# Optimization experiments

Hardware: AMD Instinct MI355X
Metric: run time of the kernel (lower is better)

## Reference

```python
import jax, jax.numpy as jnp
import numpy as np

B, F0, D = 4096, 39, 16
CROSS_LAYER_SIZE = (128, 128)


def _he_uniform(key, shape):
    fan_in = int(np.prod(shape[:-1]))
    limit = np.sqrt(6.0 / fan_in)
    return jax.random.uniform(key, shape, jnp.float32, -limit, limit)


def setup_inputs() -> dict:
    key = jax.random.key(0)
    k_x, k_f0, k_f1, k_w, k_b = jax.random.split(key, 5)
    x = jax.random.normal(k_x, (B, F0, D), dtype=jnp.float32)
    # field_nums with direct=False: [39, 128//2=64, 64]
    f0 = _he_uniform(k_f0, (F0 * F0, CROSS_LAYER_SIZE[0]))          # (1521, 128)
    f1 = _he_uniform(k_f1, (F0 * (CROSS_LAYER_SIZE[0] // 2), CROSS_LAYER_SIZE[1]))  # (2496, 128)
    out_dim = CROSS_LAYER_SIZE[0] // 2 + CROSS_LAYER_SIZE[1]        # 192
    dense_w = _he_uniform(k_w, (out_dim, 1))
    dense_b = jnp.zeros((1,), dtype=jnp.float32)
    return {"x": x, "f0": f0, "f1": f1, "dense_w": dense_w, "dense_b": dense_b}


def reference(x, f0, f1, dense_w, dense_b):
    # CIN forward (direct=False, use_bias=False, use_residual=False, relu)
    # x: (B, F0, D)
    filters = [f0, f1]
    n_layers = len(CROSS_LAYER_SIZE)
    h = x  # hidden state, (B, Fk, D)
    finals = []
    for idx, L in enumerate(CROSS_LAYER_SIZE):
        Fk = h.shape[1]
        # filter f_ has shape (F0*Fk, L) with i (field of x0) major, j (field of h) minor
        Wr = filters[idx].reshape(F0, Fk, L)
        # fused outer product + conv1d (kernel width 1 == matmul over i,j):
        # z[b, m, d] = sum_{i,j} x[b,i,d] * h[b,j,d] * W[i,j,m]
        z = jnp.einsum('bid,bjd,ijm->bmd', x, h, Wr)  # (B, L, D)
        z = jax.nn.relu(z)
        if idx != n_layers - 1:
            # split along feature-map axis: first half feeds next layer,
            # second half goes to output
            h = z[:, : L // 2, :]
            finals.append(z[:, L // 2:, :])
        else:
            finals.append(z)
    result = jnp.sum(jnp.concatenate(finals, axis=1), axis=-1)  # (B, 192)
    return result @ dense_w + dense_b  # (B, 1)
```

## Files before the change

### kernel.cpp

```cpp
#include <hip/hip_runtime.h>


typedef _Float16 h2    __attribute__((ext_vector_type(2)));
typedef _Float16 f16x8 __attribute__((ext_vector_type(8)));
typedef __attribute__((ext_vector_type(16))) float f32x16;

#define XBB 1160
#define L0C 30
#define NCH 110

__device__ __constant__ int IG0[L0C] = {0,0,0,0,0, 1,1,1,1,1, 2,2,2,2, 3,3,3,3, 4,4,4, 5,5,5, 6,6, 7,7, 8, 9};
__device__ __constant__ int JG0[L0C] = {0,1,2,3,4, 0,1,2,3,4, 1,2,3,4, 1,2,3,4, 2,3,4, 2,3,4, 3,4, 3,4, 4, 4};
#define IG0T(c) ((c)<5?0:(c)<10?1:(c)<14?2:(c)<18?3:(c)<21?4:(c)<24?5:(c)<26?6:(c)<28?7:(c)<29?8:9)
#define JG0T(c) ((c)<10?((c)%5):(c)<18?(((c)-10)%4+1):(c)<24?(((c)-18)%3+2):(c)<28?(((c)-24)%2+3):4)

__global__ __launch_bounds__(256)
void CIN_repack(const float* __restrict__ f0, const float* __restrict__ f1,
                uint4* __restrict__ ws)
{
    const int tid  = blockIdx.x * 256 + threadIdx.x;
    const int n    = tid & 127;
    const int slot = tid >> 7;
    const int half = slot & 1;
    const int kh   = (slot >> 1) & 1;
    const int ch   = slot >> 2;
    float v[8];
    if (ch < L0C) {
        const int ig = IG0[ch], jg = JG0[ch];
        const int i = ig * 4 + kh * 2 + half;
#pragma unroll
        for (int t = 0; t < 8; ++t) {
            const int j = jg * 8 + t;
            float val = 0.f;
            if (i < 39 && j < 39 && j >= i) {
                val = f0[(i * 39 + j) * 128 + n];
                if (j > i) val += f0[(j * 39 + i) * 128 + n];
            }
            v[t] = val;
        }
    } else {
        const int c1 = ch - L0C;
        const int jg = c1 / 5, ig = c1 - jg * 5;
        const int j = jg * 4 + kh * 2 + half;
#pragma unroll
        for (int t = 0; t < 8; ++t) {
            const int i = ig * 8 + t;
            v[t] = (i < 39) ? f1[(i * 64 + j) * 128 + n] : 0.f;
        }
    }
    union { h2 h[4]; uint4 q; } pk;
#pragma unroll
    for (int t = 0; t < 4; ++t)
        pk.h[t] = h2{(_Float16)v[2 * t], (_Float16)v[2 * t + 1]};
    const int lane = half * 32 + (n & 31);
    const int cg   = n >> 5;
    ws[ch * 512 + kh * 256 + cg * 64 + lane] = pk.q;
}

__global__ __launch_bounds__(256, 4)
void CIN_main(const float* __restrict__ x,
              const char* __restrict__ wsB,
              const float* __restrict__ dw,
              const float* __restrict__ db,
              float* __restrict__ out)
{
    __shared__ __align__(16) _Float16 xsH[4 * XBB];
    __shared__ __align__(4)  _Float16 hsH[4][64][18];
    __shared__ float dws[192];
    __shared__ float red[4][4];

    const int tid  = threadIdx.x;
    const int w    = tid >> 6;
    const int lane = tid & 63;
    const int half = lane >> 5;
    const int d    = lane & 15;
    const int bsel = (lane >> 4) & 1;
    const int col  = lane & 31;

    const char* wbase = wsB + lane * 16 + w * 1024 + 2048;
    f16x8 Bb[2][2];
    auto loadBg = [&](int ch, f16x8 (&B)[2]) {
        const char* p0 = wbase + (size_t)ch * 8192;
        B[0] = *(const f16x8*)(p0 - 2048);
        B[1] = *(const f16x8*)(p0 + 2048);
    };

    loadBg(0, Bb[0]);
    loadBg(1, Bb[1]);

    const float4* xg4 = (const float4*)(x + (size_t)blockIdx.x * 4 * 624);
    for (int e4 = tid; e4 < 624; e4 += 256) {
        float4 v = xg4[e4];
        int bb = e4 / 156, r = e4 - bb * 156;
        int i = r >> 2, d0 = (r & 3) * 4;
        _Float16* bp = xsH + bb * XBB + i;
        bp[(d0 + 0) * 72] = (_Float16)v.x; bp[(d0 + 1) * 72] = (_Float16)v.y;
        bp[(d0 + 2) * 72] = (_Float16)v.z; bp[(d0 + 3) * 72] = (_Float16)v.w;
    }
    if (tid < 64) { int bb = tid >> 4, dd = tid & 15; xsH[bb * XBB + dd * 72 + 39] = (_Float16)0.f; }
    if (tid < 192) dws[tid] = dw[tid];
    __syncthreads();

    const _Float16* xrow[2] = {
        xsH + (0 * 2 + bsel) * XBB + d * 72,
        xsH + (1 * 2 + bsel) * XBB + d * 72
    };

    f32x16 acc[2];
#pragma unroll
    for (int p = 0; p < 2; ++p)
#pragma unroll
        for (int r = 0; r < 16; ++r) acc[p][r] = 0.f;

    h2 xiv2[2][2];

#pragma unroll
    for (int c = 0; c < L0C; ++c) {
        const int ig = IG0T(c);
        const int jg = JG0T(c);
        if ((c == 0) || (IG0T(c) != IG0T(c - 1))) {
#pragma unroll
            for (int p = 0; p < 2; ++p)
#pragma unroll
                for (int kh = 0; kh < 2; ++kh) {
                    _Float16 s = xrow[p][ig * 4 + kh * 2 + half];
                    xiv2[p][kh] = h2{s, s};
                }
        }
#pragma unroll
        for (int p = 0; p < 2; ++p) {
            union { f16x8 v; h2 h[4]; } xj;
            xj.v = *(const f16x8*)(xrow[p] + jg * 8);
            union { h2 h[4]; f16x8 v; } a0, a1;
#pragma unroll
            for (int q = 0; q < 4; ++q) {
                a0.h[q] = xiv2[p][0] * xj.h[q];
                a1.h[q] = xiv2[p][1] * xj.h[q];
            }
            acc[p] = __builtin_amdgcn_mfma_f32_32x32x16_f16(a0.v, Bb[c & 1][0], acc[p], 0, 0, 0);
            acc[p] = __builtin_amdgcn_mfma_f32_32x32x16_f16(a1.v, Bb[c & 1][1], acc[p], 0, 0, 0);
        }
        loadBg(c + 2, Bb[c & 1]);
    }

    float cs[4] = {0.f, 0.f, 0.f, 0.f};
    if (w < 2) {
#pragma unroll
        for (int p = 0; p < 2; ++p)
#pragma unroll
            for (int r = 0; r < 16; r += 2) {
                const int row = (r & 3) + 8 * (r >> 2) + 4 * half;
                h2 pr = h2{(_Float16)fmaxf(acc[p][r],     0.f),
                           (_Float16)fmaxf(acc[p][r + 1], 0.f)};
                *(h2*)&hsH[p * 2 + (row >> 4)][w * 32 + col][row & 15] = pr;
            }
    } else {
        const float dwv = dws[(w - 2) * 32 + col];
#pragma unroll
        for (int p = 0; p < 2; ++p)
#pragma unroll
            for (int r = 0; r < 16; ++r) {
                const int row = (r & 3) + 8 * (r >> 2) + 4 * half;
                cs[p * 2 + (row >> 4)] += fmaxf(acc[p][r], 0.f) * dwv;
            }
    }
#pragma unroll
    for (int p = 0; p < 2; ++p)
#pragma unroll
        for (int r = 0; r < 16; ++r) acc[p][r] = 0.f;
    __syncthreads();

#pragma unroll 1
    for (int o2 = 0; o2 < 8; ++o2) {
#pragma unroll
        for (int u = 0; u < 10; ++u) {
            const int ch = L0C + o2 * 10 + u;
            const int ig2 = u % 5;
            if (ig2 == 0) {
                const int jb = (o2 * 2 + u / 5) * 4;
#pragma unroll
                for (int p = 0; p < 2; ++p)
#pragma unroll
                    for (int kh = 0; kh < 2; ++kh) {
                        _Float16 s = hsH[p * 2 + bsel][jb + kh * 2 + half][d];
                        xiv2[p][kh] = h2{s, s};
                    }
            }
#pragma unroll
            for (int p = 0; p < 2; ++p) {
                union { f16x8 v; h2 h[4]; } xj;
                xj.v = *(const f16x8*)(xrow[p] + ig2 * 8);
                union { h2 h[4]; f16x8 v; } a0, a1;
#pragma unroll
                for (int q = 0; q < 4; ++q) {
                    a0.h[q] = xiv2[p][0] * xj.h[q];
                    a1.h[q] = xiv2[p][1] * xj.h[q];
                }
                acc[p] = __builtin_amdgcn_mfma_f32_32x32x16_f16(a0.v, Bb[u & 1][0], acc[p], 0, 0, 0);
                acc[p] = __builtin_amdgcn_mfma_f32_32x32x16_f16(a1.v, Bb[u & 1][1], acc[p], 0, 0, 0);
            }
            int chn = ch + 2; if (chn > NCH - 1) chn = NCH - 1;
            loadBg(chn, Bb[u & 1]);
        }
    }

    {
        const float dwv = dws[64 + w * 32 + col];
#pragma unroll
        for (int p = 0; p < 2; ++p)
#pragma unroll
            for (int r = 0; r < 16; ++r) {
                const int row = (r & 3) + 8 * (r >> 2) + 4 * half;
                cs[p * 2 + (row >> 4)] += fmaxf(acc[p][r], 0.f) * dwv;
            }
    }
#pragma unroll
    for (int rr = 0; rr < 4; ++rr)
#pragma unroll
        for (int off = 32; off > 0; off >>= 1)
            cs[rr] += __shfl_xor(cs[rr], off, 64);
    if (lane == 0) {
#pragma unroll
        for (int rr = 0; rr < 4; ++rr) red[w][rr] = cs[rr];
    }
    __syncthreads();
    if (tid < 4)
        out[blockIdx.x * 4 + tid] = red[0][tid] + red[1][tid] + red[2][tid] + red[3][tid] + db[0];
}

extern "C" void kernel_launch(void* const* d_in, const int* in_sizes, int n_in,
                              void* d_out, int out_size, void* d_ws, size_t ws_size,
                              hipStream_t stream)
{
    const float* x  = (const float*)d_in[0];
    const float* f0 = (const float*)d_in[1];
    const float* f1 = (const float*)d_in[2];
    const float* dw = (const float*)d_in[3];
    const float* db = (const float*)d_in[4];
    float* out = (float*)d_out;

    CIN_repack<<<dim3(220), dim3(256), 0, stream>>>(f0, f1, (uint4*)d_ws);
    CIN_main<<<dim3(1024), dim3(256), 0, stream>>>(x, (const char*)d_ws, dw, db, out);
}
```

Measured before the change: 124.9 us.

## Split K reduction across two wave groups with LDS partial-sum combine

Doubles the block to 512 threads so two groups of four waves each take half of the K chunks in both CIN layers. The partial accumulators are summed through a new LDS buffer before ReLU and the dense reduction. The aim is more parallelism per block and shorter serial MFMA chains per wave. In exchange it adds LDS traffic, extra barriers and more LDS per block, and it drops the explicit occupancy hint.

Measured after the change: 124.1 us. No clear change (-0.6%).

```diff
diff --git a/kernel.cpp b/kernel.cpp
--- a/kernel.cpp
+++ b/kernel.cpp
@@ -57,7 +57,7 @@
     ws[ch * 512 + kh * 256 + cg * 64 + lane] = pk.q;
 }
 
-__global__ __launch_bounds__(256, 4)
+__global__ __launch_bounds__(512)
 void CIN_main(const float* __restrict__ x,
               const char* __restrict__ wsB,
               const float* __restrict__ dw,
@@ -66,11 +66,14 @@
 {
     __shared__ __align__(16) _Float16 xsH[4 * XBB];
     __shared__ __align__(4)  _Float16 hsH[4][64][18];
+    __shared__ __align__(8)  float accst[4][64][18];
     __shared__ float dws[192];
     __shared__ float red[4][4];
 
     const int tid  = threadIdx.x;
-    const int w    = tid >> 6;
+    const int wv   = tid >> 6;
+    const int w    = wv & 3;
+    const int ks   = wv >> 2;
     const int lane = tid & 63;
     const int half = lane >> 5;
     const int d    = lane & 15;
@@ -85,11 +88,11 @@
         B[1] = *(const f16x8*)(p0 + 2048);
     };
 
-    loadBg(0, Bb[0]);
-    loadBg(1, Bb[1]);
+    loadBg(ks ? 15 : 0, Bb[0]);
+    loadBg(ks ? 16 : 1, Bb[1]);
 
     const float4* xg4 = (const float4*)(x + (size_t)blockIdx.x * 4 * 624);
-    for (int e4 = tid; e4 < 624; e4 += 256) {
+    for (int e4 = tid; e4 < 624; e4 += 512) {
         float4 v = xg4[e4];
         int bb = e4 / 156, r = e4 - bb * 156;
         int i = r >> 2, d0 = (r & 3) * 4;
@@ -114,70 +117,108 @@
 
     h2 xiv2[2][2];
 
-#pragma unroll
-    for (int c = 0; c < L0C; ++c) {
-        const int ig = IG0T(c);
-        const int jg = JG0T(c);
-        if ((c == 0) || (IG0T(c) != IG0T(c - 1))) {
-#pragma unroll
-            for (int p = 0; p < 2; ++p)
-#pragma unroll
-                for (int kh = 0; kh < 2; ++kh) {
-                    _Float16 s = xrow[p][ig * 4 + kh * 2 + half];
-                    xiv2[p][kh] = h2{s, s};
+#define CHUNK_STEP(JW, PH)                                                          \
+    {                                                                               \
+        _Pragma("unroll")                                                           \
+        for (int p = 0; p < 2; ++p) {                                               \
+            union { f16x8 v; h2 h[4]; } xj;                                         \
+            xj.v = *(const f16x8*)(xrow[p] + (JW) * 8);                             \
+            union { h2 h[4]; f16x8 v; } a0, a1;                                     \
+            _Pragma("unroll")                                                       \
+            for (int q = 0; q < 4; ++q) {                                           \
+                a0.h[q] = xiv2[p][0] * xj.h[q];                                     \
+                a1.h[q] = xiv2[p][1] * xj.h[q];                                     \
+            }                                                                       \
+            acc[p] = __builtin_amdgcn_mfma_f32_32x32x16_f16(a0.v, Bb[PH][0], acc[p], 0, 0, 0); \
+            acc[p] = __builtin_amdgcn_mfma_f32_32x32x16_f16(a1.v, Bb[PH][1], acc[p], 0, 0, 0); \
+        }                                                                           \
+    }
+
+    if (ks == 0) {
+#pragma unroll
+        for (int c = 0; c < 15; ++c) {
+            const int ig = IG0T(c), jg = JG0T(c);
+            if (c == 0 || IG0T(c) != IG0T(c - 1)) {
+#pragma unroll
+                for (int p = 0; p < 2; ++p)
+#pragma unroll
+                    for (int kh = 0; kh < 2; ++kh) {
+                        _Float16 s = xrow[p][ig * 4 + kh * 2 + half];
+                        xiv2[p][kh] = h2{s, s};
+                    }
+            }
+            CHUNK_STEP(jg, c & 1)
+            const int p2 = c + 2;
+            loadBg(p2 < 15 ? p2 : 30 + (p2 - 15), Bb[c & 1]);
+        }
+    } else {
+#pragma unroll
+        for (int c = 0; c < 15; ++c) {
+            const int cc = c + 15;
+            const int ig = IG0T(cc), jg = JG0T(cc);
+            if (c == 0 || IG0T(cc) != IG0T(cc - 1)) {
+#pragma unroll
+                for (int p = 0; p < 2; ++p)
+#pragma unroll
+                    for (int kh = 0; kh < 2; ++kh) {
+                        _Float16 s = xrow[p][ig * 4 + kh * 2 + half];
+                        xiv2[p][kh] = h2{s, s};
+                    }
+            }
+            CHUNK_STEP(jg, c & 1)
+            const int p2 = c + 2;
+            loadBg(p2 < 15 ? 15 + p2 : 70 + (p2 - 15), Bb[c & 1]);
+        }
+    }
+
+    float cs[4] = {0.f, 0.f, 0.f, 0.f};
+#pragma unroll
+    for (int p = 0; p < 2; ++p) {
+        if (ks == 1) {
+            float* dst = &accst[w][lane][0];
+#pragma unroll
+            for (int r = 0; r < 16; r += 2)
+                *(float2*)(dst + r) = make_float2(acc[p][r], acc[p][r + 1]);
+        }
+        __syncthreads();
+        if (ks == 0) {
+            const float* src = &accst[w][lane][0];
+            float z[16];
+#pragma unroll
+            for (int r = 0; r < 16; ++r) z[r] = acc[p][r] + src[r];
+            if (w < 2) {
+#pragma unroll
+                for (int r = 0; r < 16; r += 2) {
+                    const int row = (r & 3) + 8 * (r >> 2) + 4 * half;
+                    h2 pr = h2{(_Float16)fmaxf(z[r],     0.f),
+                               (_Float16)fmaxf(z[r + 1], 0.f)};
+                    *(h2*)&hsH[p * 2 + (row >> 4)][w * 32 + col][row & 15] = pr;
                 }
-        }
-#pragma unroll
-        for (int p = 0; p < 2; ++p) {
-            union { f16x8 v; h2 h[4]; } xj;
-            xj.v = *(const f16x8*)(xrow[p] + jg * 8);
-            union { h2 h[4]; f16x8 v; } a0, a1;
-#pragma unroll
-            for (int q = 0; q < 4; ++q) {
-                a0.h[q] = xiv2[p][0] * xj.h[q];
-                a1.h[q] = xiv2[p][1] * xj.h[q];
-            }
-            acc[p] = __builtin_amdgcn_mfma_f32_32x32x16_f16(a0.v, Bb[c & 1][0], acc[p], 0, 0, 0);
-            acc[p] = __builtin_amdgcn_mfma_f32_32x32x16_f16(a1.v, Bb[c & 1][1], acc[p], 0, 0, 0);
-        }
-        loadBg(c + 2, Bb[c & 1]);
-    }
-
-    float cs[4] = {0.f, 0.f, 0.f, 0.f};
-    if (w < 2) {
-#pragma unroll
-        for (int p = 0; p < 2; ++p)
-#pragma unroll
-            for (int r = 0; r < 16; r += 2) {
-                const int row = (r & 3) + 8 * (r >> 2) + 4 * half;
-                h2 pr = h2{(_Float16)fmaxf(acc[p][r],     0.f),
-                           (_Float16)fmaxf(acc[p][r + 1], 0.f)};
-                *(h2*)&hsH[p * 2 + (row >> 4)][w * 32 + col][row & 15] = pr;
-            }
-    } else {
-        const float dwv = dws[(w - 2) * 32 + col];
-#pragma unroll
-        for (int p = 0; p < 2; ++p)
-#pragma unroll
-            for (int r = 0; r < 16; ++r) {
-                const int row = (r & 3) + 8 * (r >> 2) + 4 * half;
-                cs[p * 2 + (row >> 4)] += fmaxf(acc[p][r], 0.f) * dwv;
-            }
+            } else {
+                const float dwv = dws[(w - 2) * 32 + col];
+#pragma unroll
+                for (int r = 0; r < 16; ++r) {
+                    const int row = (r & 3) + 8 * (r >> 2) + 4 * half;
+                    cs[p * 2 + (row >> 4)] += fmaxf(z[r], 0.f) * dwv;
+                }
+            }
+        }
+        __syncthreads();
     }
 #pragma unroll
     for (int p = 0; p < 2; ++p)
 #pragma unroll
         for (int r = 0; r < 16; ++r) acc[p][r] = 0.f;
-    __syncthreads();
-
+
+    const int chBase = ks ? 70 : 30;
+    const int jgBase = ks * 8;
 #pragma unroll 1
-    for (int o2 = 0; o2 < 8; ++o2) {
+    for (int o2 = 0; o2 < 4; ++o2) {
 #pragma unroll
         for (int u = 0; u < 10; ++u) {
-            const int ch = L0C + o2 * 10 + u;
-            const int ig2 = u % 5;
-            if (ig2 == 0) {
-                const int jb = (o2 * 2 + u / 5) * 4;
+            const int igx = u % 5;
+            if (igx == 0) {
+                const int jb = (jgBase + o2 * 2 + u / 5) * 4;
 #pragma unroll
                 for (int p = 0; p < 2; ++p)
 #pragma unroll
@@ -186,46 +227,48 @@
                         xiv2[p][kh] = h2{s, s};
                     }
             }
-#pragma unroll
-            for (int p = 0; p < 2; ++p) {
-                union { f16x8 v; h2 h[4]; } xj;
-                xj.v = *(const f16x8*)(xrow[p] + ig2 * 8);
-                union { h2 h[4]; f16x8 v; } a0, a1;
-#pragma unroll
-                for (int q = 0; q < 4; ++q) {
-                    a0.h[q] = xiv2[p][0] * xj.h[q];
-                    a1.h[q] = xiv2[p][1] * xj.h[q];
-                }
-                acc[p] = __builtin_amdgcn_mfma_f32_32x32x16_f16(a0.v, Bb[u & 1][0], acc[p], 0, 0, 0);
-                acc[p] = __builtin_amdgcn_mfma_f32_32x32x16_f16(a1.v, Bb[u & 1][1], acc[p], 0, 0, 0);
-            }
-            int chn = ch + 2; if (chn > NCH - 1) chn = NCH - 1;
-            loadBg(chn, Bb[u & 1]);
-        }
-    }
-
-    {
-        const float dwv = dws[64 + w * 32 + col];
-#pragma unroll
-        for (int p = 0; p < 2; ++p)
+            CHUNK_STEP(igx, (u + 1) & 1)
+            int idx2 = o2 * 10 + u + 2; if (idx2 > 39) idx2 = 39;
+            loadBg(chBase + idx2, Bb[(u + 1) & 1]);
+        }
+    }
+
+#pragma unroll
+    for (int p = 0; p < 2; ++p) {
+        if (ks == 1) {
+            float* dst = &accst[w][lane][0];
+#pragma unroll
+            for (int r = 0; r < 16; r += 2)
+                *(float2*)(dst + r) = make_float2(acc[p][r], acc[p][r + 1]);
+        }
+        __syncthreads();
+        if (ks == 0) {
+            const float* src = &accst[w][lane][0];
+            const float dwv = dws[64 + w * 32 + col];
 #pragma unroll
             for (int r = 0; r < 16; ++r) {
                 const int row = (r & 3) + 8 * (r >> 2) + 4 * half;
-                cs[p * 2 + (row >> 4)] += fmaxf(acc[p][r], 0.f) * dwv;
-            }
-    }
-#pragma unroll
-    for (int rr = 0; rr < 4; ++rr)
-#pragma unroll
-        for (int off = 32; off > 0; off >>= 1)
-            cs[rr] += __shfl_xor(cs[rr], off, 64);
-    if (lane == 0) {
-#pragma unroll
-        for (int rr = 0; rr < 4; ++rr) red[w][rr] = cs[rr];
+                cs[p * 2 + (row >> 4)] += fmaxf(acc[p][r] + src[r], 0.f) * dwv;
+            }
+        }
+        __syncthreads();
+    }
+
+    if (ks == 0) {
+#pragma unroll
+        for (int rr = 0; rr < 4; ++rr)
+#pragma unroll
+            for (int off = 32; off > 0; off >>= 1)
+                cs[rr] += __shfl_xor(cs[rr], off, 64);
+        if (lane == 0) {
+#pragma unroll
+            for (int rr = 0; rr < 4; ++rr) red[w][rr] = cs[rr];
+        }
     }
     __syncthreads();
     if (tid < 4)
         out[blockIdx.x * 4 + tid] = red[0][tid] + red[1][tid] + red[2][tid] + red[3][tid] + db[0];
+#undef CHUNK_STEP
 }
 
 extern "C" void kernel_launch(void* const* d_in, const int* in_sizes, int n_in,
@@ -240,5 +283,5 @@
     float* out = (float*)d_out;
 
     CIN_repack<<<dim3(220), dim3(256), 0, stream>>>(f0, f1, (uint4*)d_ws);
-    CIN_main<<<dim3(1024), dim3(256), 0, stream>>>(x, (const char*)d_ws, dw, db, out);
+    CIN_main<<<dim3(1024), dim3(512), 0, stream>>>(x, (const char*)d_ws, dw, db, out);
 }
```
